# Optimization experiments

Hardware: AMD Instinct MI355X
Metric: run time of the kernel (lower is better)

## Reference

```python
import jax, jax.numpy as jnp
import numpy as np

KH, KW = 11, 11
H, W = 6144, 6144


def setup_inputs() -> dict:
    key = jax.random.key(0)
    k1, k2 = jax.random.split(key)
    X = jax.random.normal(k1, (H, W), dtype=jnp.float32)
    weight = jax.random.uniform(k2, (KH, KW), dtype=jnp.float32)
    bias = jnp.zeros((1,), dtype=jnp.float32)
    return {"X": X, "weight": weight, "bias": bias}


def reference(X, weight, bias):
    # valid 2D cross-correlation: out[i,j] = sum(X[i:i+kh, j:j+kw] * K) + bias
    lhs = X[None, None]            # (1, 1, H, W)
    rhs = weight[None, None]       # (1, 1, kh, kw)  cross-correlation (no flip)
    out = jax.lax.conv_general_dilated(
        lhs, rhs,
        window_strides=(1, 1),
        padding="VALID",
        dimension_numbers=("NCHW", "OIHW", "NCHW"),
    )[0, 0]                         # (H-kh+1, W-kw+1)
    return out + bias[0]
```

## Files before the change

### kernel.cpp

```cpp
#include <hip/hip_runtime.h>

typedef _Float16 half8 __attribute__((ext_vector_type(8)));
typedef __fp16  fp16x2 __attribute__((ext_vector_type(2)));
typedef float f32x4 __attribute__((ext_vector_type(4)));

#define HH 6144
#define WW 6144
#define KH 11
#define KW 11
#define OH (HH - KH + 1)
#define OW (WW - KW + 1)

#define BROWS 32
#define BCOLS 96
#define SR 42
#define SCH 28
#define F_ROWB 448
#define H_ROWB 224
#define A_TASKS 1176
#define A_WAVES 19
#define B_LDS 9408
#define B_BYTES 7168
#define LDSB 19456
#define CV_TASKS 588

#define TILES_X 64
#define TILES_Y 192
#define NWG (TILES_X * TILES_Y)

__global__ void build_B_kernel(const float* __restrict__ Wt,
                               _Float16* __restrict__ Bc) {
    const int t = (int)blockIdx.x * 256 + (int)threadIdx.x;
    if (t < 448 * 8) {
        const int e  = t & 7;
        const int p  = t >> 3;
        const int kb = p / 40;
        const int sg = p - kb * 40;
        const int s  = (sg % 5) * 8 + sg / 5;
        float v = 0.f;
        if (kb < KH) {
            const int d = s + e - 15;
            if (d >= 0 && d < KW) v = Wt[kb * KW + d];
        }
        Bc[t] = (_Float16)v;
    }
}

union pk2 { fp16x2 h; unsigned int u; };
static __device__ __forceinline__ unsigned int cvt2(float a, float b) {
#if defined(__has_builtin) && __has_builtin(__builtin_amdgcn_cvt_pkrtz)
    pk2 r; r.h = __builtin_amdgcn_cvt_pkrtz(a, b);
#else
    pk2 r; r.h[0] = (__fp16)a; r.h[1] = (__fp16)b;
#endif
    return r.u;
}

__global__ __launch_bounds__(256, 8)
void conv2d_dma8_kernel(const float* __restrict__ X,
                        const _Float16* __restrict__ Bc,
                        const float* __restrict__ bias,
                        float* __restrict__ out)
{
    __shared__ __align__(16) char lds[LDSB];

    const int bid = (int)blockIdx.x;
    const int sb  = (bid & 7) * (NWG / 8) + (bid >> 3);
    const int txt = sb % TILES_X;
    const int tyt = sb / TILES_X;

    const int x0 = txt * BCOLS;
    const int y0 = tyt * BROWS;
    const int tid = (int)threadIdx.x;
    const int lane = tid & 63;
    const int wv = tid >> 6;
    const int n  = lane & 15;
    const int h  = lane >> 4;
    const int rt = wv & 1;
    const int cs = wv >> 1;
    const float bv = bias[0];

    const bool interior = (txt < TILES_X - 1) && (tyt < TILES_Y - 1);

    if (interior) {
        #pragma unroll
        for (int k = 0; k < 5; ++k) {
            const int wabs = k * 4 + wv;
            if (wabs < A_WAVES) {
                char* ldst = lds + wabs * 1024;
                const int t = wabs * 64 + lane;
                int r = t / SCH;
                const int j = t - r * SCH;
                if (r > SR - 1) r = SR - 1;
                const void* src = (const void*)(X + (size_t)(y0 + r) * WW + (x0 + 4 * j));
                __builtin_amdgcn_global_load_lds(
                    (const __attribute__((address_space(1))) void*)src,
                    (__attribute__((address_space(3))) void*)ldst,
                    16, 0, 0);
            }
        }
    } else {
        #pragma unroll 1
        for (int k = 0; k < 5; ++k) {
            const int wabs = k * 4 + wv;
            if (wabs < A_WAVES) {
                const int t = wabs * 64 + lane;
                int r = t / SCH;
                const int j = t - r * SCH;
                if (r > SR - 1) r = SR - 1;
                const int gy = y0 + r;
                const int gx = x0 + 4 * j;
                f32x4 v = {0.f, 0.f, 0.f, 0.f};
                if (gy < HH) {
                    const float* rp = X + (size_t)gy * WW;
                    if (gx + 3 < WW) {
                        v = *reinterpret_cast<const f32x4*>(rp + gx);
                    } else {
                        if (gx + 0 < WW) v[0] = rp[gx + 0];
                        if (gx + 1 < WW) v[1] = rp[gx + 1];
                        if (gx + 2 < WW) v[2] = rp[gx + 2];
                    }
                }
                *reinterpret_cast<f32x4*>(lds + (size_t)t * 16) = v;
            }
        }
    }

    __syncthreads();

    f32x4 CV[3][2];
    #pragma unroll
    for (int it = 0; it < 3; ++it) {
        const int idx = it * 256 + tid;
        if (idx < CV_TASKS) {
            const int r = idx / 14;
            const int m = idx - r * 14;
            const char* frow = lds + (size_t)r * F_ROWB + m * 32;
            CV[it][0] = *reinterpret_cast<const f32x4*>(frow);
            CV[it][1] = *reinterpret_cast<const f32x4*>(frow + 16);
        }
    }

    __syncthreads();

    if (interior) {
        #pragma unroll
        for (int k = 0; k < 2; ++k) {
            const int wb = k * 4 + wv;
            if (wb < 7) {
                char* ldst = lds + B_LDS + wb * 1024;
                const void* src = (const void*)((const char*)Bc + (size_t)(wb * 64 + lane) * 16);
                __builtin_amdgcn_global_load_lds(
                    (const __attribute__((address_space(1))) void*)src,
                    (__attribute__((address_space(3))) void*)ldst,
                    16, 0, 0);
            }
        }
    } else {
        #pragma unroll
        for (int k = 0; k < 2; ++k) {
            const int wb = k * 4 + wv;
            if (wb < 7) {
                const int t = wb * 64 + lane;
                *reinterpret_cast<uint4*>(lds + B_LDS + (size_t)t * 16) =
                    *reinterpret_cast<const uint4*>((const char*)Bc + (size_t)t * 16);
            }
        }
    }

    #pragma unroll
    for (int it = 0; it < 3; ++it) {
        const int idx = it * 256 + tid;
        if (idx < CV_TASKS) {
            const int r = idx / 14;
            const int m = idx - r * 14;
            union { unsigned int u[4]; uint4 q; } fr;
            fr.u[0] = cvt2(CV[it][0][0], CV[it][0][1]);
            fr.u[1] = cvt2(CV[it][0][2], CV[it][0][3]);
            fr.u[2] = cvt2(CV[it][1][0], CV[it][1][1]);
            fr.u[3] = cvt2(CV[it][1][2], CV[it][1][3]);
            *reinterpret_cast<uint4*>(lds + (size_t)r * H_ROWB + m * 16) = fr.q;
        }
    }

    f32x4 acc[3];
    #pragma unroll
    for (int c = 0; c < 3; ++c) acc[c] = (f32x4){bv, bv, bv, bv};

    __syncthreads();

    const int s_log = 8 * h - n + 15;
    const int sig   = (s_log & 7) * 5 + (s_log >> 3);
    const char* abase = lds + (16 * rt + n) * H_ROWB + 96 * cs + 16 * h;
    const char* bbase = lds + B_LDS + sig * 16;
    #pragma unroll
    for (int kb = 0; kb < 11; ++kb) {
        const half8 bf = *reinterpret_cast<const half8*>(bbase + kb * 640);
        const char* arow = abase + kb * H_ROWB;
        #pragma unroll
        for (int c = 0; c < 3; ++c) {
            half8 a = *reinterpret_cast<const half8*>(arow + 32 * c);
            acc[c] = __builtin_amdgcn_mfma_f32_16x16x32_f16(a, bf, acc[c], 0, 0, 0);
        }
    }

    const int orow0 = y0 + 16 * rt + 4 * h;
    const int ocol0 = x0 + 48 * cs + n;
    if (interior) {
        #pragma unroll
        for (int r = 0; r < 4; ++r) {
            float* op = out + (size_t)(orow0 + r) * OW + ocol0;
            #pragma unroll
            for (int c = 0; c < 3; ++c)
                op[16 * c] = acc[c][r];
        }
    } else {
        #pragma unroll
        for (int r = 0; r < 4; ++r) {
            if (orow0 + r < OH) {
                float* op = out + (size_t)(orow0 + r) * OW + ocol0;
                #pragma unroll
                for (int c = 0; c < 3; ++c)
                    if (ocol0 + 16 * c < OW) op[16 * c] = acc[c][r];
            }
        }
    }
}

extern "C" void kernel_launch(void* const* d_in, const int* in_sizes, int n_in,
                              void* d_out, int out_size, void* d_ws, size_t ws_size,
                              hipStream_t stream) {
    const float* X    = (const float*)d_in[0];
    const float* Wt   = (const float*)d_in[1];
    const float* bias = (const float*)d_in[2];
    float* out        = (float*)d_out;
    _Float16* Bc      = (_Float16*)d_ws;

    build_B_kernel<<<dim3(14), dim3(256), 0, stream>>>(Wt, Bc);
    conv2d_dma8_kernel<<<dim3(NWG), dim3(256), 0, stream>>>(X, Bc, bias, out);
}
```

Before: 71.12 us.

## Double tile height to 64 rows with 512-thread workgroups

Enlarges each workgroup's output tile from 32 to 64 rows and doubles the thread count to 512, with eight waves arranged as four row tiles by two column slices. This lowers the fraction of redundant halo rows loaded per output row, cutting global input traffic and the per-tile fixed costs (weight staging, barriers). In exchange, per-block LDS grows to about 33 KB and blocks are larger, which can reduce the number of resident workgroups and change latency hiding.

Result: faster. 67.52 us, median of 3 (-5.1%).

```diff
diff --git a/kernel.cpp b/kernel.cpp
--- a/kernel.cpp
+++ b/kernel.cpp
@@ -11,21 +11,20 @@
 #define OH (HH - KH + 1)
 #define OW (WW - KW + 1)
 
-#define BROWS 32
+#define NTH 512
+#define BROWS 64
 #define BCOLS 96
-#define SR 42
+#define SR 74
 #define SCH 28
 #define F_ROWB 448
 #define H_ROWB 224
-#define A_TASKS 1176
-#define A_WAVES 19
-#define B_LDS 9408
-#define B_BYTES 7168
-#define LDSB 19456
-#define CV_TASKS 588
+#define A_WAVES 33
+#define B_LDS 16576
+#define LDSB 33792
+#define CV_TASKS 1036
 
 #define TILES_X 64
-#define TILES_Y 192
+#define TILES_Y 96
 #define NWG (TILES_X * TILES_Y)
 
 __global__ void build_B_kernel(const float* __restrict__ Wt,
@@ -56,11 +55,11 @@
     return r.u;
 }
 
-__global__ __launch_bounds__(256, 8)
-void conv2d_dma8_kernel(const float* __restrict__ X,
-                        const _Float16* __restrict__ Bc,
-                        const float* __restrict__ bias,
-                        float* __restrict__ out)
+__global__ __launch_bounds__(NTH, 8)
+void conv2d_dma11_kernel(const float* __restrict__ X,
+                         const _Float16* __restrict__ Bc,
+                         const float* __restrict__ bias,
+                         float* __restrict__ out)
 {
     __shared__ __align__(16) char lds[LDSB];
 
@@ -76,8 +75,8 @@
     const int wv = tid >> 6;
     const int n  = lane & 15;
     const int h  = lane >> 4;
-    const int rt = wv & 1;
-    const int cs = wv >> 1;
+    const int rt = wv & 3;
+    const int cs = wv >> 2;
     const float bv = bias[0];
 
     const bool interior = (txt < TILES_X - 1) && (tyt < TILES_Y - 1);
@@ -85,7 +84,7 @@
     if (interior) {
         #pragma unroll
         for (int k = 0; k < 5; ++k) {
-            const int wabs = k * 4 + wv;
+            const int wabs = k * 8 + wv;
             if (wabs < A_WAVES) {
                 char* ldst = lds + wabs * 1024;
                 const int t = wabs * 64 + lane;
@@ -102,7 +101,7 @@
     } else {
         #pragma unroll 1
         for (int k = 0; k < 5; ++k) {
-            const int wabs = k * 4 + wv;
+            const int wabs = k * 8 + wv;
             if (wabs < A_WAVES) {
                 const int t = wabs * 64 + lane;
                 int r = t / SCH;
@@ -131,7 +130,7 @@
     f32x4 CV[3][2];
     #pragma unroll
     for (int it = 0; it < 3; ++it) {
-        const int idx = it * 256 + tid;
+        const int idx = it * NTH + tid;
         if (idx < CV_TASKS) {
             const int r = idx / 14;
             const int m = idx - r * 14;
@@ -144,33 +143,25 @@
     __syncthreads();
 
     if (interior) {
-        #pragma unroll
-        for (int k = 0; k < 2; ++k) {
-            const int wb = k * 4 + wv;
-            if (wb < 7) {
-                char* ldst = lds + B_LDS + wb * 1024;
-                const void* src = (const void*)((const char*)Bc + (size_t)(wb * 64 + lane) * 16);
-                __builtin_amdgcn_global_load_lds(
-                    (const __attribute__((address_space(1))) void*)src,
-                    (__attribute__((address_space(3))) void*)ldst,
-                    16, 0, 0);
-            }
+        if (wv < 7) {
+            char* ldst = lds + B_LDS + wv * 1024;
+            const void* src = (const void*)((const char*)Bc + (size_t)(wv * 64 + lane) * 16);
+            __builtin_amdgcn_global_load_lds(
+                (const __attribute__((address_space(1))) void*)src,
+                (__attribute__((address_space(3))) void*)ldst,
+                16, 0, 0);
         }
     } else {
-        #pragma unroll
-        for (int k = 0; k < 2; ++k) {
-            const int wb = k * 4 + wv;
-            if (wb < 7) {
-                const int t = wb * 64 + lane;
-                *reinterpret_cast<uint4*>(lds + B_LDS + (size_t)t * 16) =
-                    *reinterpret_cast<const uint4*>((const char*)Bc + (size_t)t * 16);
-            }
+        if (wv < 7) {
+            const int t = wv * 64 + lane;
+            *reinterpret_cast<uint4*>(lds + B_LDS + (size_t)t * 16) =
+                *reinterpret_cast<const uint4*>((const char*)Bc + (size_t)t * 16);
         }
     }
 
     #pragma unroll
     for (int it = 0; it < 3; ++it) {
-        const int idx = it * 256 + tid;
+        const int idx = it * NTH + tid;
         if (idx < CV_TASKS) {
             const int r = idx / 14;
             const int m = idx - r * 14;
@@ -237,5 +228,5 @@
     _Float16* Bc      = (_Float16*)d_ws;
 
     build_B_kernel<<<dim3(14), dim3(256), 0, stream>>>(Wt, Bc);
-    conv2d_dma8_kernel<<<dim3(NWG), dim3(256), 0, stream>>>(X, Bc, bias, out);
-}
+    conv2d_dma11_kernel<<<dim3(NWG), dim3(NTH), 0, stream>>>(X, Bc, bias, out);
+}
```
